# Performance work log

Measured on AMD Instinct MI355X. Metric: run time of the kernel, lower is better.

## Reference

```python
import jax, jax.numpy as jnp
import numpy as np

B, S, D, H = 4, 2048, 1024, 16
DK = D // H


def setup_inputs() -> dict:
    key = jax.random.key(0)
    ks = jax.random.split(key, 16)
    s = 0.02
    inp = {
        "Q": jax.random.normal(ks[0], (B, S, D), jnp.float32),
        "K": jax.random.normal(ks[1], (B, S, D), jnp.float32),
        "V": jax.random.normal(ks[2], (B, S, D), jnp.float32),
        "mask": jax.random.randint(ks[3], (B, 1, S, S), 0, 2, jnp.int32),
        "wq": jax.random.normal(ks[4], (D, D), jnp.float32) * s,
        "bq": jnp.zeros((D,), jnp.float32),
        "wk": jax.random.normal(ks[5], (D, D), jnp.float32) * s,
        "bk": jnp.zeros((D,), jnp.float32),
        "wv": jax.random.normal(ks[6], (D, D), jnp.float32) * s,
        "bv": jnp.zeros((D,), jnp.float32),
        "wo": jax.random.normal(ks[7], (D, D), jnp.float32) * s,
        "bo": jnp.zeros((D,), jnp.float32),
        "na_q_w": jax.random.normal(ks[8], (DK, DK), jnp.float32) * 0.1,
        "na_q_b": jnp.zeros((DK,), jnp.float32),
        "na_k_w": jax.random.normal(ks[9], (DK, DK), jnp.float32) * 0.1,
        "na_k_b": jnp.zeros((DK,), jnp.float32),
        "temperature": jnp.ones((H, 1, 1), jnp.float32),
        "rms_w": jnp.ones((D,), jnp.float32),
    }
    return inp


def _split_heads(x):
    # [B,S,D] -> [B,H,S,DK]
    return x.reshape(B, S, H, DK).transpose(0, 2, 1, 3)


def reference(Q, K, V, mask, wq, bq, wk, bk, wv, bv, wo, bo,
              na_q_w, na_q_b, na_k_w, na_k_b, temperature, rms_w):
    q = _split_heads(Q @ wq.T + bq)
    k = _split_heads(K @ wk.T + bk)
    v = _split_heads(V @ wv.T + bv)
    # NeuralAttention: tanh-transformed Q,K then scaled dot product
    qn = jnp.tanh(q @ na_q_w.T + na_q_b)
    kn = jnp.tanh(k @ na_k_w.T + na_k_b)
    scores = jnp.einsum("bhqd,bhkd->bhqk", qn, kn) / (DK ** 0.5)
    scores = scores / temperature  # [H,1,1] broadcasts over [B,H,S,S]
    scores = jnp.where(mask == 0, jnp.float32(-1e9), scores)
    attn = jax.nn.softmax(scores, axis=-1)
    ctx = jnp.einsum("bhqk,bhkd->bhqd", attn, v)
    out = ctx.transpose(0, 2, 1, 3).reshape(B, S, D) @ wo.T + bo
    # RMSNorm
    out = out * jax.lax.rsqrt(jnp.mean(out * out, axis=-1, keepdims=True) + 1e-8) * rms_w
    return out
```

## Files before the change

### kernel.cpp

```cpp
#include <hip/hip_runtime.h>
#include <hip/hip_bf16.h>

constexpr int Bc  = 4;
constexpr int Sc  = 2048;
constexpr int Dc  = 1024;
constexpr int Hc  = 16;
constexpr int DKc = 64;
constexpr int Mc  = Bc * Sc;

typedef __bf16 bf16x8 __attribute__((ext_vector_type(8)));
typedef float  f32x4  __attribute__((ext_vector_type(4)));
typedef unsigned short ushort_t;

#define DEV __device__ __forceinline__

DEV unsigned short f2bf(float f) {
    unsigned u = __builtin_bit_cast(unsigned, f);
    u += 0x7FFFu + ((u >> 16) & 1u);
    return (unsigned short)(u >> 16);
}
DEV unsigned pack2(float a, float b) {
    return (unsigned)f2bf(a) | ((unsigned)f2bf(b) << 16);
}
DEV void gl16(const void* g, void* l) {
    __builtin_amdgcn_global_load_lds((const __attribute__((address_space(1))) unsigned int*)g,
                                     (__attribute__((address_space(3))) unsigned int*)l, 16, 0, 0);
}
DEV f32x4 mfma16(bf16x8 a, bf16x8 b, f32x4 c) {
    return __builtin_amdgcn_mfma_f32_16x16x32_bf16(a, b, c, 0, 0, 0);
}


__global__ __launch_bounds__(256) void fold_w2(const float* __restrict__ naqw,
                                               const float* __restrict__ wq,
                                               unsigned short* __restrict__ wqf,
                                               const float* __restrict__ nakw,
                                               const float* __restrict__ wk,
                                               unsigned short* __restrict__ wkf,
                                               const float* __restrict__ bq,
                                               const float* __restrict__ naqb,
                                               float* __restrict__ bqf,
                                               const float* __restrict__ bk,
                                               const float* __restrict__ nakb,
                                               float* __restrict__ bkf) {
    const int colg = blockIdx.x, h = blockIdx.y, z = blockIdx.z;
    if (z == 2) {
        if (h >= 2) return;
        const float* na = h ? nakw : naqw;
        const float* b  = h ? bk : bq;
        const float* nb = h ? nakb : naqb;
        float* out      = h ? bkf : bqf;
        int idx = colg * 256 + threadIdx.x;
        if (idx >= Dc) return;
        int hh = idx >> 6, i = idx & 63;
        float acc = nb[i];
        for (int t = 0; t < DKc; ++t) acc += na[i * DKc + t] * b[hh * DKc + t];
        out[idx] = acc;
        return;
    }
    const float* na = z ? nakw : naqw;
    const float* w  = z ? wk : wq;
    unsigned short* out = z ? wkf : wqf;
    const int col = colg * 256 + threadIdx.x;

    __shared__ float nal[64 * 64];
    for (int i = threadIdx.x; i < 4096; i += 256) nal[i] = na[i];

    float wr[64];
#pragma unroll
    for (int t = 0; t < 64; ++t) wr[t] = w[(h * 64 + t) * Dc + col];
    __syncthreads();

    for (int i = 0; i < 64; ++i) {
        float acc = 0.f;
#pragma unroll
        for (int t = 0; t < 64; ++t) acc += nal[i * 64 + t] * wr[t];
        out[(h * 64 + i) * Dc + col] = f2bf(acc);
    }
}

__global__ __launch_bounds__(256) void conv_all(const float* __restrict__ Q,
                                                const float* __restrict__ K,
                                                const float* __restrict__ V,
                                                const float* __restrict__ wv,
                                                const float* __restrict__ wo,
                                                ushort_t* __restrict__ qb,
                                                ushort_t* __restrict__ kb,
                                                ushort_t* __restrict__ vb,
                                                ushort_t* __restrict__ wvf,
                                                ushort_t* __restrict__ wof) {
    size_t i = ((size_t)blockIdx.x * 256 + threadIdx.x) * 8;
    constexpr size_t N = (size_t)Mc * Dc;
    constexpr size_t W = (size_t)Dc * Dc;
    const float* src; ushort_t* dst; size_t off;
    if      (i < N)         { src = Q;  dst = qb;  off = i; }
    else if (i < 2 * N)     { src = K;  dst = kb;  off = i - N; }
    else if (i < 3 * N)     { src = V;  dst = vb;  off = i - 2 * N; }
    else if (i < 3 * N + W) { src = wv; dst = wvf; off = i - 3 * N; }
    else                    { src = wo; dst = wof; off = i - 3 * N - W; }
    float4 a = *(const float4*)(src + off), b = *(const float4*)(src + off + 4);
    uint4 o;
    o.x = pack2(a.x, a.y); o.y = pack2(a.z, a.w);
    o.z = pack2(b.x, b.y); o.w = pack2(b.z, b.w);
    *(uint4*)(dst + off) = o;
}

__global__ __launch_bounds__(256) void pack_mask(const int* __restrict__ m,
                                                 unsigned* __restrict__ out) {
    size_t gid = (size_t)blockIdx.x * 256 + threadIdx.x;
    int p = threadIdx.x & 63;
    int nat = (((p >> 4) & 1) << 5) | (((p >> 2) & 3) << 3) | (((p >> 5) & 1) << 2) | (p & 3);
    int v = m[(gid & ~(size_t)63) | nat];
    unsigned long long bal = __ballot(v != 0);
    int lane = threadIdx.x & 63;
    if (lane == 0)       out[gid >> 5] = (unsigned)bal;
    else if (lane == 32) out[gid >> 5] = (unsigned)(bal >> 32);
}

template <int EPI, int SWZ>
__global__ __launch_bounds__(256) void gemm_bt(const ushort_t* __restrict__ A,
                                               const ushort_t* __restrict__ B,
                                               const float* __restrict__ bias,
                                               void* __restrict__ outp,
                                               int Mdim, int Ndim, int Kdim,
                                               const float* __restrict__ temp) {
    __shared__ __align__(16) unsigned char As[2][16384];
    __shared__ __align__(16) unsigned char Bs[2][16384];

    int bx = blockIdx.x, by = blockIdx.y;
    if constexpr (SWZ != 0) {
        int nwg = gridDim.x * gridDim.y;
        int L = by * gridDim.x + bx;
        int cpx = nwg >> 3;
        int orig = (L & 7) * cpx + (L >> 3);
        if constexpr (SWZ == 1) { bx = orig % gridDim.x; by = orig / gridDim.x; }
        else                    { by = orig % gridDim.y; bx = orig / gridDim.y; }
    }

    const int tid = threadIdx.x, lane = tid & 63, wave = tid >> 6;
    const int wr = wave >> 1, wc = wave & 1;
    const int q = lane & 15, g = lane >> 4;
    const int m0 = by * 128, n0 = bx * 128;

    const int strow = lane >> 3, stcol = (lane & 7) * 8;
    const ushort_t* Ab = A + (size_t)(m0 + strow) * Kdim + stcol;
    const ushort_t* Bb = B + (size_t)(n0 + strow) * Kdim + stcol;

    f32x4 acc[4][4] = {};
    const int nK = Kdim >> 6;

#pragma unroll
    for (int i = 0; i < 4; ++i) {
        const int ro = (wave * 4 + i) * 8;
        gl16(Ab + (size_t)ro * Kdim, As[0] + (wave * 4 + i) * 1024);
        gl16(Bb + (size_t)ro * Kdim, Bs[0] + (wave * 4 + i) * 1024);
    }
    __syncthreads();

    for (int kt = 0; kt < nK; ++kt) {
        const int cur = kt & 1;
        if (kt + 1 < nK) {
            const int k1 = (kt + 1) << 6;
#pragma unroll
            for (int i = 0; i < 4; ++i) {
                const int ro = (wave * 4 + i) * 8;
                gl16(Ab + (size_t)ro * Kdim + k1, As[cur ^ 1] + (wave * 4 + i) * 1024);
                gl16(Bb + (size_t)ro * Kdim + k1, Bs[cur ^ 1] + (wave * 4 + i) * 1024);
            }
        }
#pragma unroll
        for (int s = 0; s < 2; ++s) {
            const int cb = s * 64 + g * 16;
            bf16x8 a[4], b[4];
#pragma unroll
            for (int m = 0; m < 4; ++m)
                a[m] = *(const bf16x8*)(As[cur] + (wr * 64 + m * 16 + q) * 128 + cb);
#pragma unroll
            for (int n = 0; n < 4; ++n)
                b[n] = *(const bf16x8*)(Bs[cur] + (wc * 64 + n * 16 + q) * 128 + cb);
#pragma unroll
            for (int m = 0; m < 4; ++m)
#pragma unroll
                for (int n = 0; n < 4; ++n)
                    acc[m][n] = mfma16(a[m], b[n], acc[m][n]);
        }
        __syncthreads();
    }

#pragma unroll
    for (int m = 0; m < 4; ++m)
#pragma unroll
        for (int n = 0; n < 4; ++n) {
            int gn = n0 + wc * 64 + n * 16 + q;
            float sc_h = 1.f;
            if constexpr (EPI == 0) {
                sc_h = 0.18033688011112042f * __builtin_amdgcn_rcpf(temp[gn >> 6]);
            }
#pragma unroll
            for (int r = 0; r < 4; ++r) {
                int gm = m0 + wr * 64 + m * 16 + (g << 2) + r;
                float v = acc[m][n][r];
                if constexpr (EPI == 0) {
                    v = tanhf(v + bias[gn]) * sc_h;
                    int b = gm >> 11, s = gm & 2047, hh = gn >> 6, dk = gn & 63;
                    ((unsigned short*)outp)[(((size_t)(b * Hc + hh)) * Sc + s) * DKc + dk] = f2bf(v);
                } else if constexpr (EPI == 3) {
                    v = tanhf(v + bias[gn]);
                    int b = gm >> 11, s = gm & 2047, hh = gn >> 6, dk = gn & 63;
                    int kt2 = s >> 7, nr = s & 127;
                    int prow = (nr & 64) | (((nr >> 5) & 1) << 4) | (((nr >> 3) & 3) << 2)
                             | (((nr >> 2) & 1) << 5) | (nr & 3);
                    int eofs = ((dk * 2) ^ ((prow & 7) << 4)) >> 1;
                    size_t idx = ((size_t)(b * Hc + hh)) * Sc * DKc + (size_t)kt2 * 8192 + prow * 64 + eofs;
                    ((unsigned short*)outp)[idx] = f2bf(v);
                } else if constexpr (EPI == 1) {
                    v += bias[gm];
                    int hh = gm >> 6, dk = gm & 63, b = gn >> 11, s = gn & 2047;
                    int kt2 = s >> 7, kloc = s & 127;
                    int eofs = ((kloc * 2) ^ ((dk & 7) << 4)) >> 1;
                    size_t idx = ((size_t)(b * Hc + hh)) * Sc * DKc + (size_t)kt2 * 8192 + dk * 128 + eofs;
                    ((unsigned short*)outp)[idx] = f2bf(v);
                } else {
                    v += bias[gn];
                    ((float*)outp)[(size_t)gm * Ndim + gn] = v;
                }
            }
        }
}

__global__ __launch_bounds__(512, 2) void attn_k(const ushort_t* __restrict__ qn,
                                                 const ushort_t* __restrict__ kn,
                                                 const ushort_t* __restrict__ vtp,
                                                 const unsigned* __restrict__ mbits,
                                                 ushort_t* __restrict__ ctxb) {
    __shared__ __align__(16) unsigned char Kl[2][16384];
    __shared__ __align__(16) unsigned char Vl[2][16384];

    const int tid = threadIdx.x, lane = tid & 63, wave = tid >> 6;
    const int q = lane & 15, g = lane >> 4;

    const int wg = blockIdx.x;
    const int orig = (wg & 7) * 64 + (wg >> 3);
    const int qt = orig & 7, h = (orig >> 3) & 15, b = orig >> 7;
    const int q0 = qt * 256;
    const int qr0 = q0 + wave * 32 + q;
    const size_t headoff = ((size_t)(b * Hc + h)) * Sc * DKc;

    const unsigned char* Ksrc = (const unsigned char*)(kn + headoff);
    const unsigned char* Vsrc = (const unsigned char*)(vtp + headoff);
    const int so = wave * 1024 + lane * 16;
    const int ld = wave * 1024;

    bf16x8 qf[2][2];
    {
        const ushort_t* p0 = qn + headoff + (size_t)qr0 * DKc + g * 8;
        qf[0][0] = *(const bf16x8*)p0;
        qf[0][1] = *(const bf16x8*)(p0 + 32);
        qf[1][0] = *(const bf16x8*)(p0 + 16 * DKc);
        qf[1][1] = *(const bf16x8*)(p0 + 16 * DKc + 32);
    }
    const unsigned* mr0 = mbits + ((size_t)b * Sc + qr0) * (Sc / 32);
    const unsigned* mr1 = mr0 + 16 * (Sc / 32);

    bf16x8 ones;
#pragma unroll
    for (int i = 0; i < 8; ++i) ones[i] = (__bf16)1.0f;

    f32x4 ctxa[2][4] = {};
    f32x4 lacc[2] = {};
    const int swz = (q & 7) << 4;
    const int sh = g << 2;

    gl16(Ksrc + so,        &Kl[0][ld]);
    gl16(Ksrc + 8192 + so, &Kl[0][8192 + ld]);
    gl16(Vsrc + so,        &Vl[0][ld]);
    gl16(Vsrc + 8192 + so, &Vl[0][8192 + ld]);
    __syncthreads();

    for (int kt = 0; kt < Sc / 128; ++kt) {
        const int cur = kt & 1;
        if (kt < Sc / 128 - 1) {
            const unsigned char* ks = Ksrc + (kt + 1) * 16384;
            const unsigned char* vs = Vsrc + (kt + 1) * 16384;
            gl16(ks + so,        &Kl[cur ^ 1][ld]);
            gl16(ks + 8192 + so, &Kl[cur ^ 1][8192 + ld]);
            gl16(vs + so,        &Vl[cur ^ 1][ld]);
            gl16(vs + 8192 + so, &Vl[cur ^ 1][8192 + ld]);
        }
        unsigned mwq[2][4];
        {
            uint4 t0 = *(const uint4*)(mr0 + kt * 4);
            uint4 t1 = *(const uint4*)(mr1 + kt * 4);
            mwq[0][0] = t0.x >> sh; mwq[0][1] = t0.y >> sh;
            mwq[0][2] = t0.z >> sh; mwq[0][3] = t0.w >> sh;
            mwq[1][0] = t1.x >> sh; mwq[1][1] = t1.y >> sh;
            mwq[1][2] = t1.z >> sh; mwq[1][3] = t1.w >> sh;
        }
        const unsigned char* Kb = Kl[cur];
        const unsigned char* Vb = Vl[cur];

#pragma unroll
        for (int kh = 0; kh < 2; ++kh) {
            f32x4 s0[4] = {}, s1[4] = {};
            __builtin_amdgcn_s_setprio(1);
#pragma unroll
            for (int f = 0; f < 4; ++f) {
                const int ro = (kh * 64 + f * 16 + q) * 128;
                bf16x8 a0 = *(const bf16x8*)(Kb + ro + ((g * 16) ^ swz));
                bf16x8 a1 = *(const bf16x8*)(Kb + ro + ((64 + g * 16) ^ swz));
                s0[f] = mfma16(a0, qf[0][0], s0[f]);
                s0[f] = mfma16(a1, qf[0][1], s0[f]);
                s1[f] = mfma16(a0, qf[1][0], s1[f]);
                s1[f] = mfma16(a1, qf[1][1], s1[f]);
            }
            __builtin_amdgcn_s_setprio(0);

#pragma unroll
            for (int f = 0; f < 4; ++f) {
                unsigned w0 = mwq[0][kh * 2 + (f >> 1)];
                unsigned w1 = mwq[1][kh * 2 + (f >> 1)];
#pragma unroll
                for (int r = 0; r < 4; ++r) {
                    const unsigned bitc = 1u << (((f & 1) << 4) + r);
                    float v0 = (w0 & bitc) ? s0[f][r] : -1e30f;
                    float v1 = (w1 & bitc) ? s1[f][r] : -1e30f;
                    s0[f][r] = __builtin_amdgcn_exp2f(v0);
                    s1[f][r] = __builtin_amdgcn_exp2f(v1);
                }
            }

            bf16x8 pa0[2], pa1[2];
#pragma unroll
            for (int cs = 0; cs < 2; ++cs)
#pragma unroll
                for (int r = 0; r < 4; ++r) {
                    pa0[cs][r]     = (__bf16)s0[cs][r];
                    pa0[cs][4 + r] = (__bf16)s0[cs + 2][r];
                    pa1[cs][r]     = (__bf16)s1[cs][r];
                    pa1[cs][4 + r] = (__bf16)s1[cs + 2][r];
                }

            __builtin_amdgcn_s_setprio(1);
#pragma unroll
            for (int cs = 0; cs < 2; ++cs) {
                const int csg = kh * 2 + cs;
                lacc[0] = mfma16(pa0[cs], ones, lacc[0]);
                lacc[1] = mfma16(pa1[cs], ones, lacc[1]);
#pragma unroll
                for (int j = 0; j < 4; ++j) {
                    bf16x8 vb = *(const bf16x8*)(Vb + (j * 16 + q) * 256 + ((csg * 64 + g * 16) ^ swz));
                    ctxa[0][j] = mfma16(pa0[cs], vb, ctxa[0][j]);
                    ctxa[1][j] = mfma16(pa1[cs], vb, ctxa[1][j]);
                }
            }
            __builtin_amdgcn_s_setprio(0);
        }
        __syncthreads();
    }

#pragma unroll
    for (int qg = 0; qg < 2; ++qg) {
        f32x4 linv;
#pragma unroll
        for (int r = 0; r < 4; ++r) linv[r] = __builtin_amdgcn_rcpf(lacc[qg][r]);
#pragma unroll
        for (int j = 0; j < 4; ++j)
#pragma unroll
            for (int r = 0; r < 4; ++r) {
                int srow = q0 + wave * 32 + qg * 16 + (g << 2) + r;
                int col = h * DKc + j * 16 + q;
                float v = ctxa[qg][j][r] * linv[r];
                ctxb[((size_t)b * Sc + srow) * Dc + col] = __builtin_bit_cast(unsigned short, (__bf16)v);
            }
    }
}

__global__ __launch_bounds__(256) void rmsnorm_k(float* __restrict__ out,
                                                 const float* __restrict__ w) {
    const int row = blockIdx.x, tid = threadIdx.x;
    float4* p = (float4*)(out + (size_t)row * Dc) + tid;
    float4 v = *p;
    float ss = v.x * v.x + v.y * v.y + v.z * v.z + v.w * v.w;
#pragma unroll
    for (int o = 32; o >= 1; o >>= 1) ss += __shfl_xor(ss, o);
    __shared__ float sm[4];
    if ((tid & 63) == 0) sm[tid >> 6] = ss;
    __syncthreads();
    float tot = sm[0] + sm[1] + sm[2] + sm[3];
    float r = rsqrtf(tot * (1.f / Dc) + 1e-8f);
    float4 wv = *((const float4*)w + tid);
    v.x *= r * wv.x; v.y *= r * wv.y; v.z *= r * wv.z; v.w *= r * wv.w;
    *p = v;
}

extern "C" void kernel_launch(void* const* d_in, const int* in_sizes, int n_in,
                              void* d_out, int out_size, void* d_ws, size_t ws_size,
                              hipStream_t stream) {
    (void)in_sizes; (void)n_in; (void)out_size; (void)ws_size;
    const float* Q    = (const float*)d_in[0];
    const float* K    = (const float*)d_in[1];
    const float* V    = (const float*)d_in[2];
    const int*   mask = (const int*)  d_in[3];
    const float* wq   = (const float*)d_in[4];
    const float* bq   = (const float*)d_in[5];
    const float* wk   = (const float*)d_in[6];
    const float* bk   = (const float*)d_in[7];
    const float* wv   = (const float*)d_in[8];
    const float* bv   = (const float*)d_in[9];
    const float* wo   = (const float*)d_in[10];
    const float* bo   = (const float*)d_in[11];
    const float* naqw = (const float*)d_in[12];
    const float* naqb = (const float*)d_in[13];
    const float* nakw = (const float*)d_in[14];
    const float* nakb = (const float*)d_in[15];
    const float* temp = (const float*)d_in[16];
    const float* rmsw = (const float*)d_in[17];

    char* ws = (char*)d_ws;
    size_t off = 0;
    auto take = [&](size_t n) { char* p = ws + off; off += (n + 255) & ~(size_t)255; return p; };
    unsigned short* vtb  = (unsigned short*)take((size_t)Mc * Dc * 2);
    unsigned short* qb   = (unsigned short*)take((size_t)Mc * Dc * 2);
    unsigned short* kb   = (unsigned short*)take((size_t)Mc * Dc * 2);
    unsigned short* vb   = (unsigned short*)take((size_t)Mc * Dc * 2);
    unsigned short* wqf  = (unsigned short*)take((size_t)Dc * Dc * 2);
    unsigned short* wkf  = (unsigned short*)take((size_t)Dc * Dc * 2);
    unsigned short* wvf  = (unsigned short*)take((size_t)Dc * Dc * 2);
    unsigned short* wof  = (unsigned short*)take((size_t)Dc * Dc * 2);
    float*    bqf   = (float*)take(Dc * 4);
    float*    bkf   = (float*)take(Dc * 4);
    unsigned* mbits = (unsigned*)take((size_t)Bc * Sc * (Sc / 32) * 4);
    unsigned short* qnb  = vb;
    unsigned short* knb  = qb;
    unsigned short* ctxb = kb;

    fold_w2<<<dim3(4, 16, 3), 256, 0, stream>>>(naqw, wq, wqf, nakw, wk, wkf,
                                                bq, naqb, bqf, bk, nakb, bkf);
    conv_all<<<dim3((3 * Mc * Dc + 2 * Dc * Dc) / 8 / 256), 256, 0, stream>>>(
        Q, K, V, wv, wo, qb, kb, vb, wvf, wof);
    pack_mask<<<dim3(Bc * Sc * Sc / 256), 256, 0, stream>>>(mask, mbits);

    gemm_bt<1, 2><<<dim3(Mc / 128, Dc / 128), 256, 0, stream>>>(
        wvf, vb, bv, vtb, Dc, Mc, Dc, nullptr);
    gemm_bt<0, 1><<<dim3(Dc / 128, Mc / 128), 256, 0, stream>>>(
        qb, wqf, bqf, qnb, Mc, Dc, Dc, temp);
    gemm_bt<3, 1><<<dim3(Dc / 128, Mc / 128), 256, 0, stream>>>(
        kb, wkf, bkf, knb, Mc, Dc, Dc, nullptr);

    attn_k<<<dim3(512), 512, 0, stream>>>(qnb, knb, vtb, mbits, ctxb);

    gemm_bt<2, 1><<<dim3(Dc / 128, Mc / 128), 256, 0, stream>>>(
        ctxb, wof, bo, d_out, Mc, Dc, Dc, nullptr);
    rmsnorm_k<<<dim3(Mc), 256, 0, stream>>>((float*)d_out, rmsw);
}
```

Before: 307.0 us.

## Enlarge GEMM tiles to 256x128 with 512 threads and fuse convert/mask kernels

```diff
diff --git a/kernel.cpp b/kernel.cpp
--- a/kernel.cpp
+++ b/kernel.cpp
@@ -79,52 +79,56 @@
     }
 }
 
-__global__ __launch_bounds__(256) void conv_all(const float* __restrict__ Q,
-                                                const float* __restrict__ K,
-                                                const float* __restrict__ V,
-                                                const float* __restrict__ wv,
-                                                const float* __restrict__ wo,
-                                                ushort_t* __restrict__ qb,
-                                                ushort_t* __restrict__ kb,
-                                                ushort_t* __restrict__ vb,
-                                                ushort_t* __restrict__ wvf,
-                                                ushort_t* __restrict__ wof) {
-    size_t i = ((size_t)blockIdx.x * 256 + threadIdx.x) * 8;
-    constexpr size_t N = (size_t)Mc * Dc;
-    constexpr size_t W = (size_t)Dc * Dc;
-    const float* src; ushort_t* dst; size_t off;
-    if      (i < N)         { src = Q;  dst = qb;  off = i; }
-    else if (i < 2 * N)     { src = K;  dst = kb;  off = i - N; }
-    else if (i < 3 * N)     { src = V;  dst = vb;  off = i - 2 * N; }
-    else if (i < 3 * N + W) { src = wv; dst = wvf; off = i - 3 * N; }
-    else                    { src = wo; dst = wof; off = i - 3 * N - W; }
-    float4 a = *(const float4*)(src + off), b = *(const float4*)(src + off + 4);
-    uint4 o;
-    o.x = pack2(a.x, a.y); o.y = pack2(a.z, a.w);
-    o.z = pack2(b.x, b.y); o.w = pack2(b.z, b.w);
-    *(uint4*)(dst + off) = o;
-}
-
-__global__ __launch_bounds__(256) void pack_mask(const int* __restrict__ m,
-                                                 unsigned* __restrict__ out) {
-    size_t gid = (size_t)blockIdx.x * 256 + threadIdx.x;
-    int p = threadIdx.x & 63;
-    int nat = (((p >> 4) & 1) << 5) | (((p >> 2) & 3) << 3) | (((p >> 5) & 1) << 2) | (p & 3);
-    int v = m[(gid & ~(size_t)63) | nat];
-    unsigned long long bal = __ballot(v != 0);
-    int lane = threadIdx.x & 63;
-    if (lane == 0)       out[gid >> 5] = (unsigned)bal;
-    else if (lane == 32) out[gid >> 5] = (unsigned)(bal >> 32);
+constexpr int CONVB = (3 * Mc * Dc + 2 * Dc * Dc) / 8 / 256;
+constexpr int MASKB = Bc * Sc * Sc / 256;
+__global__ __launch_bounds__(256) void conv_mask(const float* __restrict__ Q,
+                                                 const float* __restrict__ K,
+                                                 const float* __restrict__ V,
+                                                 const float* __restrict__ wv,
+                                                 const float* __restrict__ wo,
+                                                 ushort_t* __restrict__ qb,
+                                                 ushort_t* __restrict__ kb,
+                                                 ushort_t* __restrict__ vb,
+                                                 ushort_t* __restrict__ wvf,
+                                                 ushort_t* __restrict__ wof,
+                                                 const int* __restrict__ m,
+                                                 unsigned* __restrict__ mbits) {
+    const int bid = blockIdx.x;
+    if (bid < CONVB) {
+        size_t i = ((size_t)bid * 256 + threadIdx.x) * 8;
+        constexpr size_t N = (size_t)Mc * Dc;
+        constexpr size_t W = (size_t)Dc * Dc;
+        const float* src; ushort_t* dst; size_t off;
+        if      (i < N)         { src = Q;  dst = qb;  off = i; }
+        else if (i < 2 * N)     { src = K;  dst = kb;  off = i - N; }
+        else if (i < 3 * N)     { src = V;  dst = vb;  off = i - 2 * N; }
+        else if (i < 3 * N + W) { src = wv; dst = wvf; off = i - 3 * N; }
+        else                    { src = wo; dst = wof; off = i - 3 * N - W; }
+        float4 a = *(const float4*)(src + off), b = *(const float4*)(src + off + 4);
+        uint4 o;
+        o.x = pack2(a.x, a.y); o.y = pack2(a.z, a.w);
+        o.z = pack2(b.x, b.y); o.w = pack2(b.z, b.w);
+        *(uint4*)(dst + off) = o;
+    } else {
+        size_t gid = (size_t)(bid - CONVB) * 256 + threadIdx.x;
+        int p = threadIdx.x & 63;
+        int nat = (((p >> 4) & 1) << 5) | (((p >> 2) & 3) << 3) | (((p >> 5) & 1) << 2) | (p & 3);
+        int v = m[(gid & ~(size_t)63) | nat];
+        unsigned long long bal = __ballot(v != 0);
+        int lane = threadIdx.x & 63;
+        if (lane == 0)       mbits[gid >> 5] = (unsigned)bal;
+        else if (lane == 32) mbits[gid >> 5] = (unsigned)(bal >> 32);
+    }
 }
 
 template <int EPI, int SWZ>
-__global__ __launch_bounds__(256) void gemm_bt(const ushort_t* __restrict__ A,
+__global__ __launch_bounds__(512) void gemm_bt(const ushort_t* __restrict__ A,
                                                const ushort_t* __restrict__ B,
                                                const float* __restrict__ bias,
                                                void* __restrict__ outp,
                                                int Mdim, int Ndim, int Kdim,
                                                const float* __restrict__ temp) {
-    __shared__ __align__(16) unsigned char As[2][16384];
+    __shared__ __align__(16) unsigned char As[2][32768];
     __shared__ __align__(16) unsigned char Bs[2][16384];
 
     int bx = blockIdx.x, by = blockIdx.y;
@@ -140,7 +144,7 @@
     const int tid = threadIdx.x, lane = tid & 63, wave = tid >> 6;
     const int wr = wave >> 1, wc = wave & 1;
     const int q = lane & 15, g = lane >> 4;
-    const int m0 = by * 128, n0 = bx * 128;
+    const int m0 = by * 256, n0 = bx * 128;
 
     const int strow = lane >> 3, stcol = (lane & 7) * 8;
     const ushort_t* Ab = A + (size_t)(m0 + strow) * Kdim + stcol;
@@ -149,25 +153,26 @@
     f32x4 acc[4][4] = {};
     const int nK = Kdim >> 6;
 
-#pragma unroll
-    for (int i = 0; i < 4; ++i) {
-        const int ro = (wave * 4 + i) * 8;
-        gl16(Ab + (size_t)ro * Kdim, As[0] + (wave * 4 + i) * 1024);
-        gl16(Bb + (size_t)ro * Kdim, Bs[0] + (wave * 4 + i) * 1024);
-    }
+#define STAGE(buf, k0)                                                          \
+    {                                                                           \
+        _Pragma("unroll")                                                       \
+        for (int i = 0; i < 4; ++i) {                                           \
+            const int ro = (wave * 4 + i) * 8;                                  \
+            gl16(Ab + (size_t)ro * Kdim + (k0), As[buf] + (wave * 4 + i) * 1024); \
+        }                                                                       \
+        _Pragma("unroll")                                                       \
+        for (int i = 0; i < 2; ++i) {                                           \
+            const int ro = (wave * 2 + i) * 8;                                  \
+            gl16(Bb + (size_t)ro * Kdim + (k0), Bs[buf] + (wave * 2 + i) * 1024); \
+        }                                                                       \
+    }
+
+    STAGE(0, 0);
     __syncthreads();
 
     for (int kt = 0; kt < nK; ++kt) {
         const int cur = kt & 1;
-        if (kt + 1 < nK) {
-            const int k1 = (kt + 1) << 6;
-#pragma unroll
-            for (int i = 0; i < 4; ++i) {
-                const int ro = (wave * 4 + i) * 8;
-                gl16(Ab + (size_t)ro * Kdim + k1, As[cur ^ 1] + (wave * 4 + i) * 1024);
-                gl16(Bb + (size_t)ro * Kdim + k1, Bs[cur ^ 1] + (wave * 4 + i) * 1024);
-            }
-        }
+        if (kt + 1 < nK) STAGE(cur ^ 1, (kt + 1) << 6);
 #pragma unroll
         for (int s = 0; s < 2; ++s) {
             const int cb = s * 64 + g * 16;
@@ -186,6 +191,7 @@
         }
         __syncthreads();
     }
+#undef STAGE
 
 #pragma unroll
     for (int m = 0; m < 4; ++m)
@@ -436,20 +442,20 @@
 
     fold_w2<<<dim3(4, 16, 3), 256, 0, stream>>>(naqw, wq, wqf, nakw, wk, wkf,
                                                 bq, naqb, bqf, bk, nakb, bkf);
-    conv_all<<<dim3((3 * Mc * Dc + 2 * Dc * Dc) / 8 / 256), 256, 0, stream>>>(
-        Q, K, V, wv, wo, qb, kb, vb, wvf, wof);
-    pack_mask<<<dim3(Bc * Sc * Sc / 256), 256, 0, stream>>>(mask, mbits);
-
-    gemm_bt<1, 2><<<dim3(Mc / 128, Dc / 128), 256, 0, stream>>>(
+    conv_mask<<<dim3(CONVB + MASKB), 256, 0, stream>>>(Q, K, V, wv, wo,
+                                                       qb, kb, vb, wvf, wof,
+                                                       mask, mbits);
+
+    gemm_bt<1, 2><<<dim3(Mc / 128, Dc / 256), 512, 0, stream>>>(
         wvf, vb, bv, vtb, Dc, Mc, Dc, nullptr);
-    gemm_bt<0, 1><<<dim3(Dc / 128, Mc / 128), 256, 0, stream>>>(
+    gemm_bt<0, 1><<<dim3(Dc / 128, Mc / 256), 512, 0, stream>>>(
         qb, wqf, bqf, qnb, Mc, Dc, Dc, temp);
-    gemm_bt<3, 1><<<dim3(Dc / 128, Mc / 128), 256, 0, stream>>>(
+    gemm_bt<3, 1><<<dim3(Dc / 128, Mc / 256), 512, 0, stream>>>(
         kb, wkf, bkf, knb, Mc, Dc, Dc, nullptr);
 
     attn_k<<<dim3(512), 512, 0, stream>>>(qnb, knb, vtb, mbits, ctxb);
 
-    gemm_bt<2, 1><<<dim3(Dc / 128, Mc / 128), 256, 0, stream>>>(
+    gemm_bt<2, 1><<<dim3(Dc / 128, Mc / 256), 512, 0, stream>>>(
         ctxb, wof, bo, d_out, Mc, Dc, Dc, nullptr);
     rmsnorm_k<<<dim3(Mc), 256, 0, stream>>>((float*)d_out, rmsw);
 }
```

Measured after the change: 312.1 us. About the same (+1.6%).
